# Kernel tuning notes

Measured on AMD Instinct MI355X. Metric: run time of the kernel, lower is better.

## Reference

```python
import jax, jax.numpy as jnp
import numpy as np

NUM_HEAD = 8


def setup_inputs() -> dict:
    key = jax.random.key(0)
    ks = jax.random.split(key, 4)
    B, nd, nh, nw, N, C = 1, 4, 4, 4, 512, 512
    x = jax.random.normal(ks[0], (B, nd, nh, nw, N, C), dtype=jnp.float32)
    w_qkv = jax.random.normal(ks[1], (C, 3 * C), dtype=jnp.float32) / np.sqrt(C).astype(np.float32)
    b_qkv = jnp.zeros((3 * C,), dtype=jnp.float32)
    w_proj = jax.random.normal(ks[2], (C, C), dtype=jnp.float32) / np.sqrt(C).astype(np.float32)
    b_proj = jnp.zeros((C,), dtype=jnp.float32)
    return {"x": x, "w_qkv": w_qkv, "b_qkv": b_qkv, "w_proj": w_proj, "b_proj": b_proj}


def reference(x, w_qkv, b_qkv, w_proj, b_proj):
    B, nd, nh, nw, N, C = x.shape
    hd = C // NUM_HEAD
    # QKV projection, split into q/k/v with per-head layout [B,nd,nh,nw,N,H,hd]
    qkv = (x @ w_qkv + b_qkv).reshape(B, nd, nh, nw, N, 3, NUM_HEAD, hd)
    q = qkv[..., 0, :, :]
    k = qkv[..., 1, :, :]
    v = qkv[..., 2, :, :]
    # Block-local attention. NOTE: original module defines self.scale but never
    # applies it in forward, so no 1/sqrt(hd) scaling here (faithful to source).
    attn = jnp.einsum('...qhd,...khd->...hqk', q, k)  # [B,nd,nh,nw,H,N,N]
    attn = jax.nn.softmax(attn, axis=-1)
    out = jnp.einsum('...hqk,...khd->...qhd', attn, v)  # [B,nd,nh,nw,N,H,hd]
    out = out.reshape(B, nd, nh, nw, N, C)
    return out @ w_proj + b_proj
```

## Files before the change

kernel.cpp:

```cpp
#include <hip/hip_runtime.h>
#include <hip/hip_bf16.h>

typedef _Float16 half8_t __attribute__((ext_vector_type(8)));
typedef _Float16 half4_t __attribute__((ext_vector_type(4)));
typedef _Float16 half2_t __attribute__((ext_vector_type(2)));
typedef float    f32x4   __attribute__((ext_vector_type(4)));
typedef float    f32x16  __attribute__((ext_vector_type(16)));

#define CDIM 512
#define NHEAD 8
#define HD 64
#define NTOK 512
#define NWIN 64
#define TC 1536

__device__ __forceinline__ float fexp2(float x) {
  float r;
  asm("v_exp_f32 %0, %1" : "=v"(r) : "v"(x));
  return r;
}

#define GLL16(g, l)                                                        \
  __builtin_amdgcn_global_load_lds((const __attribute__((address_space(1))) void*)(g), \
                                   (__attribute__((address_space(3))) void*)(l), 16, 0, 0)


__global__ __launch_bounds__(256) void cvt_x(const float* __restrict__ x,
                                             _Float16* __restrict__ x16, int n8) {
  int idx = blockIdx.x * 256 + threadIdx.x;
  if (idx < n8) {
    int row = (idx * 8) >> 9;
    int k = (idx * 8) & 511;
    const float4 v0 = *(const float4*)(x + (size_t)row * 512 + k);
    const float4 v1 = *(const float4*)(x + (size_t)row * 512 + k + 4);
    half8_t hv = {(_Float16)v0.x, (_Float16)v0.y, (_Float16)v0.z, (_Float16)v0.w,
                  (_Float16)v1.x, (_Float16)v1.y, (_Float16)v1.z, (_Float16)v1.w};
    *(half8_t*)(x16 + (size_t)(row >> 4) * 8192 + (size_t)(k >> 5) * 512 +
                (row & 15) * 32 + ((k & 31) >> 3) * 8) = hv;
  }
}

__global__ __launch_bounds__(256) void prep_weights(
    const float* __restrict__ wqkv, const float* __restrict__ wproj,
    _Float16* __restrict__ wqkvT, _Float16* __restrict__ wprojT) {
  __shared__ _Float16 T[64 * 65];
  int b = blockIdx.x;
  const float* src; _Float16* dst; int Cc, r0, c0; bool blocked;
  if (b < 192) {
    src = wqkv; dst = wqkvT; Cc = 1536; blocked = true;
    c0 = (b % 24) * 64; r0 = (b / 24) * 64;
  } else {
    b -= 192; src = wproj; dst = wprojT; Cc = 512; blocked = false;
    c0 = (b & 7) * 64; r0 = (b >> 3) * 64;
  }
  const int t = threadIdx.x;
#pragma unroll
  for (int i = 0; i < 16; ++i) {
    int idx = i * 256 + t, rr = idx >> 6, cc = idx & 63;
    T[rr * 65 + cc] = (_Float16)src[(size_t)(r0 + rr) * Cc + c0 + cc];
  }
  __syncthreads();
#pragma unroll
  for (int i = 0; i < 2; ++i) {
    int idx = i * 256 + t, ol = idx >> 3, c8 = idx & 7;
    half8_t vv;
#pragma unroll
    for (int e = 0; e < 8; ++e) vv[e] = T[(c8 * 8 + e) * 65 + ol];
    int o = c0 + ol, k = r0 + c8 * 8;
    if (blocked)
      *(half8_t*)(dst + (size_t)(o >> 4) * 8192 + (size_t)(k >> 5) * 512 +
                  (o & 15) * 32 + ((k & 31) >> 3) * 8) = vv;
    else
      *(half8_t*)(dst + (size_t)o * 512 + k) = vv;
  }
}

__global__ __launch_bounds__(256, 3) void gemm1_qkv(
    const _Float16* __restrict__ x16,
    const _Float16* __restrict__ wT,
    const float* __restrict__ bias,
    _Float16* __restrict__ qkv) {
  __shared__ __align__(16) char ring[3 * 16384];
  char* ringB = ring;
  const int tid = threadIdx.x;
  const int l = tid & 63;
  const int wid = tid >> 6;
  const int wr = wid >> 1, wc = wid & 1;
  const int lr = l & 15, g = l >> 4;
  const int koff = ((g ^ ((lr >> 1) & 3)) << 4);
  const int m0 = blockIdx.x * 128;
  const int cb = blockIdx.y * 128;
  const int j = cb >> 9;

  const int r4 = l >> 2;
  const int schk = (l & 3) ^ ((r4 >> 1) & 3);
  const size_t laneT = (size_t)r4 * 64 + (size_t)schk * 16;
  const size_t aTile = ((size_t)(blockIdx.x * 8 + wid * 2)) * 16384 + laneT;
  const size_t bTile = ((size_t)(blockIdx.y * 8 + wid * 2)) * 16384 + laneT;

#define ISSUE_G1(KS)                                                              \
  {                                                                               \
    char* sa = ringB + ((KS) % 3) * 16384;                                        \
    char* sbB = sa + 8192;                                                        \
    _Pragma("unroll") for (int i = 0; i < 2; ++i) {                               \
      GLL16((const char*)x16 + aTile + (size_t)i * 16384 + (size_t)(KS)*1024,     \
            sa + wid * 2048 + i * 1024);                                          \
      GLL16((const char*)wT + bTile + (size_t)i * 16384 + (size_t)(KS)*1024,      \
            sbB + wid * 2048 + i * 1024);                                         \
    }                                                                             \
  }

  ISSUE_G1(0) ISSUE_G1(1)

  f32x4 acc[4][4] = {};

#define GITER(KS, NW)                                                             \
  {                                                                               \
    asm volatile("s_waitcnt vmcnt(" NW ")" ::: "memory");                         \
    __builtin_amdgcn_sched_barrier(0);                                            \
    asm volatile("s_barrier" ::: "memory");                                       \
    if ((KS) + 2 < 16) ISSUE_G1((KS) + 2)                                         \
    char* sa = ringB + ((KS) % 3) * 16384;                                        \
    char* sbB = sa + 8192;                                                        \
    half8_t a[4], b[4];                                                           \
    _Pragma("unroll") for (int mt = 0; mt < 4; ++mt)                              \
        a[mt] = *(const half8_t*)(sa + (wr * 64 + mt * 16 + lr) * 64 + koff);     \
    _Pragma("unroll") for (int nt = 0; nt < 4; ++nt)                              \
        b[nt] = *(const half8_t*)(sbB + (wc * 64 + nt * 16 + lr) * 64 + koff);    \
    __builtin_amdgcn_s_setprio(1);                                                \
    _Pragma("unroll") for (int mt = 0; mt < 4; ++mt)                              \
        _Pragma("unroll") for (int nt = 0; nt < 4; ++nt)                          \
            acc[mt][nt] =                                                         \
                __builtin_amdgcn_mfma_f32_16x16x32_f16(a[mt], b[nt], acc[mt][nt], 0, 0, 0); \
    __builtin_amdgcn_s_setprio(0);                                                \
  }

  GITER(0, "4")  GITER(1, "4")  GITER(2, "4")  GITER(3, "4")
  GITER(4, "4")  GITER(5, "4")  GITER(6, "4")  GITER(7, "4")
  GITER(8, "4")  GITER(9, "4")  GITER(10, "4") GITER(11, "4")
  GITER(12, "4") GITER(13, "4") GITER(14, "4") GITER(15, "0")

  if (j == 2) {
#pragma unroll
    for (int nt = 0; nt < 4; ++nt) {
      const int ch = cb + wc * 64 + nt * 16 + lr;
      const int h = (ch >> 6) & 7, d = ch & 63;
      const float bvs = bias[ch];
#pragma unroll
      for (int mt = 0; mt < 4; ++mt) {
        const int row = m0 + wr * 64 + mt * 16 + g * 4;
        const int wL = row >> 9, n = row & 511;
        _Float16* panel = qkv + ((size_t)(wL * 24 + 16 + h) << 15);
        const int kg = n >> 4, hh = (n >> 2) & 1, e4 = (n & 8) >> 1;
        half4_t pk = {(_Float16)(acc[mt][nt][0] + bvs), (_Float16)(acc[mt][nt][1] + bvs),
                      (_Float16)(acc[mt][nt][2] + bvs), (_Float16)(acc[mt][nt][3] + bvs)};
        *(half4_t*)(panel + ((size_t)(kg * 2 + hh) * 64 + d) * 8 + e4) = pk;
      }
    }
  } else {
    __syncthreads();
    const float scl = (j == 0) ? 1.44269504f : 1.0f;
    char* CB = ringB;
#pragma unroll
    for (int nt = 0; nt < 4; ++nt) {
      const int chl = wc * 64 + nt * 16 + lr;
      const float bvs = bias[cb + chl];
#pragma unroll
      for (int mt = 0; mt < 4; ++mt) {
#pragma unroll
        for (int r = 0; r < 4; ++r) {
          int nl = wr * 64 + mt * 16 + g * 4 + r;
          *(_Float16*)(CB + nl * 256 + ((chl * 2) ^ ((nl & 7) << 5))) =
              (_Float16)((acc[mt][nt][r] + bvs) * scl);
        }
      }
    }
    __syncthreads();
#pragma unroll
    for (int i = 0; i < 8; ++i) {
      int idx = i * 256 + tid, nl = idx >> 4, c8 = idx & 15;
      half8_t vv = *(const half8_t*)(CB + nl * 256 + ((c8 * 16) ^ ((nl & 7) << 5)));
      int chg = cb + c8 * 8;
      int h = (chg >> 6) & 7, d = chg & 63;
      int ng = m0 + nl, wL = ng >> 9, nn = ng & 511;
      _Float16* panel = qkv + ((size_t)(wL * 24 + j * 8 + h) << 15);
      *(half8_t*)(panel + (size_t)nn * 64 + d) = vv;
    }
  }
}

__global__ __launch_bounds__(512) void attn_win(_Float16* __restrict__ qkv) {
  __shared__ __align__(16) char ring[4 * 8192];
  char* ringB = ring;
  const int tid = threadIdx.x;
  const int l = tid & 63;
  const int wid = tid >> 6;
  const int q32 = l & 31;
  const int h2 = l >> 5;
  const int wh = blockIdx.x;
  const int qc = blockIdx.y;
  const int h = wh & 7;
  const int w = wh >> 3;
  _Float16* Qp = qkv + ((size_t)(w * 24 + h) << 15);
  const _Float16* Kp = qkv + ((size_t)(w * 24 + 8 + h) << 15);
  const _Float16* Vp = qkv + ((size_t)(w * 24 + 16 + h) << 15);
  const int qrow = qc * 256 + wid * 32 + q32;

  const size_t kSrc = (size_t)(l >> 3) * 128 + (size_t)((l & 7) ^ (l >> 3)) * 16;
  const int kof0 = ((0 * 2 + h2) ^ (q32 & 7)) << 4;
  const int kof1 = ((1 * 2 + h2) ^ (q32 & 7)) << 4;
  const int kof2 = ((2 * 2 + h2) ^ (q32 & 7)) << 4;
  const int kof3 = ((3 * 2 + h2) ^ (q32 & 7)) << 4;
  const int voff = 4096 + h2 * 1024 + q32 * 16;

#define ISSUE_SLOT(KT)                                                            \
  {                                                                               \
    char* sb = ringB + ((KT)&3) * 8192;                                           \
    if (wid < 4) {                                                                \
      GLL16((const char*)Kp + (size_t)(KT)*4096 + (size_t)wid * 1024 + kSrc,      \
            sb + wid * 1024);                                                     \
    } else {                                                                      \
      GLL16((const char*)Vp + (size_t)(KT)*4096 + (size_t)(wid - 4) * 1024 + l * 16, \
            sb + 4096 + (wid - 4) * 1024);                                        \
    }                                                                             \
  }

  half8_t qf[4];
#pragma unroll
  for (int j = 0; j < 4; ++j)
    qf[j] = *(const half8_t*)(Qp + (size_t)qrow * 64 + j * 16 + h2 * 8);
  asm volatile("s_waitcnt vmcnt(0)" ::: "memory");

  ISSUE_SLOT(0) ISSUE_SLOT(1) ISSUE_SLOT(2)

  f32x16 o0 = {}, o1 = {};
  float m_run = -1e30f, lsum = 0.f;

#define AITER(KT, NW)                                                             \
  {                                                                               \
    asm volatile("s_waitcnt vmcnt(" NW ")" ::: "memory");                         \
    __builtin_amdgcn_sched_barrier(0);                                            \
    asm volatile("s_barrier" ::: "memory");                                       \
    if ((KT) + 3 < 16) ISSUE_SLOT((KT) + 3)                                       \
    char* sl = ringB + ((KT)&3) * 8192;                                           \
    half8_t kf0 = *(const half8_t*)(sl + q32 * 128 + kof0);                       \
    half8_t kf1 = *(const half8_t*)(sl + q32 * 128 + kof1);                       \
    half8_t kf2 = *(const half8_t*)(sl + q32 * 128 + kof2);                       \
    half8_t kf3 = *(const half8_t*)(sl + q32 * 128 + kof3);                       \
    __builtin_amdgcn_s_setprio(1);                                                \
    f32x16 s = {};                                                                \
    s = __builtin_amdgcn_mfma_f32_32x32x16_f16(kf0, qf[0], s, 0, 0, 0);           \
    s = __builtin_amdgcn_mfma_f32_32x32x16_f16(kf1, qf[1], s, 0, 0, 0);           \
    s = __builtin_amdgcn_mfma_f32_32x32x16_f16(kf2, qf[2], s, 0, 0, 0);           \
    s = __builtin_amdgcn_mfma_f32_32x32x16_f16(kf3, qf[3], s, 0, 0, 0);           \
    __builtin_amdgcn_s_setprio(0);                                                \
    float ma = fmaxf(fmaxf(s[0], s[1]), s[2]);                                    \
    float mb = fmaxf(fmaxf(s[3], s[4]), s[5]);                                    \
    float mc = fmaxf(fmaxf(s[6], s[7]), s[8]);                                    \
    float md = fmaxf(fmaxf(s[9], s[10]), s[11]);                                  \
    float me = fmaxf(fmaxf(s[12], s[13]), s[14]);                                 \
    float mf_ = fmaxf(fmaxf(ma, mb), mc);                                         \
    float mg = fmaxf(fmaxf(md, me), s[15]);                                       \
    float tmax = fmaxf(mf_, mg);                                                  \
    tmax = fmaxf(tmax, __shfl_xor(tmax, 32));                                     \
    if (!__all(tmax <= m_run + 11.5f)) {                                          \
      float mNew = fmaxf(m_run, tmax);                                            \
      float sc = fexp2(m_run - mNew);                                             \
      lsum *= sc;                                                                 \
      _Pragma("unroll") for (int r = 0; r < 16; ++r) { o0[r] *= sc; o1[r] *= sc; }\
      m_run = mNew;                                                               \
    }                                                                             \
    half8_t pf0, pf1;                                                             \
    float tsum = 0.f;                                                             \
    _Pragma("unroll") for (int e = 0; e < 4; ++e) {                               \
      float a0 = fexp2(s[2 * e] - m_run), a1 = fexp2(s[2 * e + 1] - m_run);       \
      tsum += a0 + a1;                                                            \
      ((half2_t*)&pf0)[e] =                                                       \
          __builtin_bit_cast(half2_t, __builtin_amdgcn_cvt_pkrtz(a0, a1));        \
    }                                                                             \
    _Pragma("unroll") for (int e = 0; e < 4; ++e) {                               \
      float a0 = fexp2(s[8 + 2 * e] - m_run), a1 = fexp2(s[9 + 2 * e] - m_run);   \
      tsum += a0 + a1;                                                            \
      ((half2_t*)&pf1)[e] =                                                       \
          __builtin_bit_cast(half2_t, __builtin_amdgcn_cvt_pkrtz(a0, a1));        \
    }                                                                             \
    tsum += __shfl_xor(tsum, 32);                                                 \
    lsum += tsum;                                                                 \
    half8_t vf0 = *(const half8_t*)(sl + voff);                                   \
    half8_t vf1 = *(const half8_t*)(sl + voff + 512);                             \
    half8_t vf2 = *(const half8_t*)(sl + voff + 2048);                            \
    half8_t vf3 = *(const half8_t*)(sl + voff + 2560);                            \
    __builtin_amdgcn_s_setprio(1);                                                \
    o0 = __builtin_amdgcn_mfma_f32_32x32x16_f16(vf0, pf0, o0, 0, 0, 0);           \
    o1 = __builtin_amdgcn_mfma_f32_32x32x16_f16(vf1, pf0, o1, 0, 0, 0);           \
    o0 = __builtin_amdgcn_mfma_f32_32x32x16_f16(vf2, pf1, o0, 0, 0, 0);           \
    o1 = __builtin_amdgcn_mfma_f32_32x32x16_f16(vf3, pf1, o1, 0, 0, 0);           \
    __builtin_amdgcn_s_setprio(0);                                                \
  }

  AITER(0, "2")  AITER(1, "2")  AITER(2, "2")  AITER(3, "2")
  AITER(4, "2")  AITER(5, "2")  AITER(6, "2")  AITER(7, "2")
  AITER(8, "2")  AITER(9, "2")  AITER(10, "2") AITER(11, "2")
  AITER(12, "2") AITER(13, "2") AITER(14, "1") AITER(15, "0")

  const float inv = 1.0f / lsum;
#pragma unroll
  for (int rq = 0; rq < 4; ++rq) {
    half4_t v0, v1;
#pragma unroll
    for (int i = 0; i < 4; ++i) {
      v0[i] = (_Float16)(o0[rq * 4 + i] * inv);
      v1[i] = (_Float16)(o1[rq * 4 + i] * inv);
    }
    *(half4_t*)(Qp + (size_t)qrow * 64 + 8 * rq + 4 * h2) = v0;
    *(half4_t*)(Qp + (size_t)qrow * 64 + 32 + 8 * rq + 4 * h2) = v1;
  }
}

__global__ __launch_bounds__(256) void gemm2_proj(
    const _Float16* __restrict__ qkv,
    const _Float16* __restrict__ wpT,
    const float* __restrict__ bias,
    float* __restrict__ out) {
  const int tid = threadIdx.x, l = tid & 63;
  const int wid = tid >> 6, wr = wid >> 1, wc = wid & 1;
  const int lr = l & 15, lk8 = (l >> 4) * 8;
  const int m0 = blockIdx.x * 128, n0 = blockIdx.y * 128;
  size_t aBase[4];
#pragma unroll
  for (int mt = 0; mt < 4; ++mt) {
    int row = m0 + wr * 64 + mt * 16 + lr;
    int wL = row >> 9, n = row & 511;
    aBase[mt] = ((size_t)(wL * 24) << 15) + (size_t)n * 64 + lk8;
  }
  size_t bBase[4];
#pragma unroll
  for (int nt = 0; nt < 4; ++nt)
    bBase[nt] = (size_t)(n0 + wc * 64 + nt * 16 + lr) * 512 + lk8;

  half8_t a[4], b[4];
#pragma unroll
  for (int mt = 0; mt < 4; ++mt) a[mt] = *(const half8_t*)(qkv + aBase[mt]);
#pragma unroll
  for (int nt = 0; nt < 4; ++nt) b[nt] = *(const half8_t*)(wpT + bBase[nt]);

  f32x4 acc[4][4] = {};
#pragma unroll 2
  for (int ks = 0; ks < 16; ++ks) {
    half8_t an[4], bn[4];
    if (ks < 15) {
      const size_t aoff = (size_t)((ks + 1) >> 1) * 32768 + (size_t)((ks + 1) & 1) * 32;
#pragma unroll
      for (int mt = 0; mt < 4; ++mt) an[mt] = *(const half8_t*)(qkv + aBase[mt] + aoff);
#pragma unroll
      for (int nt = 0; nt < 4; ++nt) bn[nt] = *(const half8_t*)(wpT + bBase[nt] + (ks + 1) * 32);
    }
#pragma unroll
    for (int mt = 0; mt < 4; ++mt)
#pragma unroll
      for (int nt = 0; nt < 4; ++nt)
        acc[mt][nt] = __builtin_amdgcn_mfma_f32_16x16x32_f16(a[mt], b[nt], acc[mt][nt], 0, 0, 0);
#pragma unroll
    for (int i = 0; i < 4; ++i) { a[i] = an[i]; b[i] = bn[i]; }
  }
#pragma unroll
  for (int nt = 0; nt < 4; ++nt) {
    int col = n0 + wc * 64 + nt * 16 + lr;
    float bv = bias[col];
#pragma unroll
    for (int mt = 0; mt < 4; ++mt) {
      int row = m0 + wr * 64 + mt * 16 + ((l >> 4) << 2);
#pragma unroll
      for (int r = 0; r < 4; ++r)
        out[(size_t)(row + r) * 512 + col] = acc[mt][nt][r] + bv;
    }
  }
}

extern "C" void kernel_launch(void* const* d_in, const int* in_sizes, int n_in,
                              void* d_out, int out_size, void* d_ws, size_t ws_size,
                              hipStream_t stream) {
  const float* x = (const float*)d_in[0];
  const float* wqkv = (const float*)d_in[1];
  const float* bqkv = (const float*)d_in[2];
  const float* wproj = (const float*)d_in[3];
  const float* bproj = (const float*)d_in[4];
  float* out = (float*)d_out;

  _Float16* wqkvT = (_Float16*)d_ws;
  _Float16* wprojT = wqkvT + (size_t)TC * CDIM;
  _Float16* chunkws = wprojT + (size_t)CDIM * CDIM;
  const size_t fixed = ((size_t)TC * CDIM + (size_t)CDIM * CDIM) * sizeof(_Float16);
  const size_t perwin = ((size_t)NTOK * CDIM + (size_t)24 * 32768) * sizeof(_Float16);
  int nw = 64;
  while (nw > 1 && fixed + (size_t)nw * perwin > ws_size) nw >>= 1;

  prep_weights<<<dim3(256), 256, 0, stream>>>(wqkv, wproj, wqkvT, wprojT);
  for (int wbase = 0; wbase < NWIN; wbase += nw) {
    const float* xc = x + (size_t)wbase * NTOK * CDIM;
    float* oc = out + (size_t)wbase * NTOK * CDIM;
    _Float16* x16 = chunkws;
    _Float16* qkvws = chunkws + (size_t)nw * NTOK * CDIM;
    const int n8 = nw * NTOK * CDIM / 8;
    cvt_x<<<dim3((n8 + 255) / 256), 256, 0, stream>>>(xc, x16, n8);
    gemm1_qkv<<<dim3(nw * 4, 12), 256, 0, stream>>>(x16, wqkvT, bqkv, qkvws);
    attn_win<<<dim3(nw * 8, 2), 512, 0, stream>>>(qkvws);
    gemm2_proj<<<dim3(nw * 4, 4), 256, 0, stream>>>(qkvws, wprojT, bproj, oc);
  }
}
```

Measured before the change: 222.3 us.

## Process two query tiles per wave in attention; restructure x conversion per row block

The attention kernel now has each wave handle 64 query rows (two 32-row tiles) across the full 512-query window. This halves the grid and reuses each K/V LDS fragment for twice as many MFMAs, which halves redundant K/V loads per window. The cost is doubled accumulator register pressure and fewer blocks to fill the GPU (512 instead of 1024). The x conversion kernel is also remapped so each block converts one 16-row slab with a loop.

```diff
diff --git a/kernel.cpp b/kernel.cpp
--- a/kernel.cpp
+++ b/kernel.cpp
@@ -26,17 +26,20 @@
 
 
 __global__ __launch_bounds__(256) void cvt_x(const float* __restrict__ x,
-                                             _Float16* __restrict__ x16, int n8) {
-  int idx = blockIdx.x * 256 + threadIdx.x;
-  if (idx < n8) {
-    int row = (idx * 8) >> 9;
-    int k = (idx * 8) & 511;
-    const float4 v0 = *(const float4*)(x + (size_t)row * 512 + k);
-    const float4 v1 = *(const float4*)(x + (size_t)row * 512 + k + 4);
+                                             _Float16* __restrict__ x16) {
+  const int rb = blockIdx.x;
+  const int l = threadIdx.x & 63, wv = threadIdx.x >> 6;
+  const int r4 = l >> 2, c = l & 3;
+  const float* src = x + (size_t)rb * 16 * 512 + (size_t)r4 * 512;
+  _Float16* dst = x16 + (size_t)rb * 8192;
+#pragma unroll
+  for (int i = 0; i < 4; ++i) {
+    int ks = wv * 4 + i;
+    const float4 v0 = *(const float4*)(src + ks * 32 + c * 8);
+    const float4 v1 = *(const float4*)(src + ks * 32 + c * 8 + 4);
     half8_t hv = {(_Float16)v0.x, (_Float16)v0.y, (_Float16)v0.z, (_Float16)v0.w,
                   (_Float16)v1.x, (_Float16)v1.y, (_Float16)v1.z, (_Float16)v1.w};
-    *(half8_t*)(x16 + (size_t)(row >> 4) * 8192 + (size_t)(k >> 5) * 512 +
-                (row & 15) * 32 + ((k & 31) >> 3) * 8) = hv;
+    *(half8_t*)(dst + ks * 512 + r4 * 32 + c * 8) = hv;
   }
 }
 
@@ -198,13 +201,13 @@
   const int q32 = l & 31;
   const int h2 = l >> 5;
   const int wh = blockIdx.x;
-  const int qc = blockIdx.y;
   const int h = wh & 7;
   const int w = wh >> 3;
   _Float16* Qp = qkv + ((size_t)(w * 24 + h) << 15);
   const _Float16* Kp = qkv + ((size_t)(w * 24 + 8 + h) << 15);
   const _Float16* Vp = qkv + ((size_t)(w * 24 + 16 + h) << 15);
-  const int qrow = qc * 256 + wid * 32 + q32;
+  const int qrowA = wid * 64 + q32;
+  const int qrowB = qrowA + 32;
 
   const size_t kSrc = (size_t)(l >> 3) * 128 + (size_t)((l & 7) ^ (l >> 3)) * 16;
   const int kof0 = ((0 * 2 + h2) ^ (q32 & 7)) << 4;
@@ -225,16 +228,28 @@
     }                                                                             \
   }
 
-  half8_t qf[4];
-#pragma unroll
-  for (int j = 0; j < 4; ++j)
-    qf[j] = *(const half8_t*)(Qp + (size_t)qrow * 64 + j * 16 + h2 * 8);
+  half8_t qfA0, qfA1, qfA2, qfA3, qfB0, qfB1, qfB2, qfB3;
+  qfA0 = *(const half8_t*)(Qp + (size_t)qrowA * 64 + 0 * 16 + h2 * 8);
+  qfA1 = *(const half8_t*)(Qp + (size_t)qrowA * 64 + 1 * 16 + h2 * 8);
+  qfA2 = *(const half8_t*)(Qp + (size_t)qrowA * 64 + 2 * 16 + h2 * 8);
+  qfA3 = *(const half8_t*)(Qp + (size_t)qrowA * 64 + 3 * 16 + h2 * 8);
+  qfB0 = *(const half8_t*)(Qp + (size_t)qrowB * 64 + 0 * 16 + h2 * 8);
+  qfB1 = *(const half8_t*)(Qp + (size_t)qrowB * 64 + 1 * 16 + h2 * 8);
+  qfB2 = *(const half8_t*)(Qp + (size_t)qrowB * 64 + 2 * 16 + h2 * 8);
+  qfB3 = *(const half8_t*)(Qp + (size_t)qrowB * 64 + 3 * 16 + h2 * 8);
   asm volatile("s_waitcnt vmcnt(0)" ::: "memory");
 
   ISSUE_SLOT(0) ISSUE_SLOT(1) ISSUE_SLOT(2)
 
-  f32x16 o0 = {}, o1 = {};
-  float m_run = -1e30f, lsum = 0.f;
+  f32x16 oA0 = {}, oA1 = {}, oB0 = {}, oB1 = {};
+  float mA = -1e30f, lsA = 0.f, mB = -1e30f, lsB = 0.f;
+
+#define SMAX(s)                                                                   \
+  fmaxf(fmaxf(fmaxf(fmaxf(fmaxf(s[0], s[1]), s[2]),                               \
+                    fmaxf(fmaxf(s[3], s[4]), s[5])),                              \
+              fmaxf(fmaxf(s[6], s[7]), s[8])),                                    \
+        fmaxf(fmaxf(fmaxf(s[9], s[10]), s[11]),                                   \
+              fmaxf(fmaxf(s[12], s[13]), fmaxf(s[14], s[15]))))
 
 #define AITER(KT, NW)                                                             \
   {                                                                               \
@@ -248,53 +263,77 @@
     half8_t kf2 = *(const half8_t*)(sl + q32 * 128 + kof2);                       \
     half8_t kf3 = *(const half8_t*)(sl + q32 * 128 + kof3);                       \
     __builtin_amdgcn_s_setprio(1);                                                \
-    f32x16 s = {};                                                                \
-    s = __builtin_amdgcn_mfma_f32_32x32x16_f16(kf0, qf[0], s, 0, 0, 0);           \
-    s = __builtin_amdgcn_mfma_f32_32x32x16_f16(kf1, qf[1], s, 0, 0, 0);           \
-    s = __builtin_amdgcn_mfma_f32_32x32x16_f16(kf2, qf[2], s, 0, 0, 0);           \
-    s = __builtin_amdgcn_mfma_f32_32x32x16_f16(kf3, qf[3], s, 0, 0, 0);           \
+    f32x16 sA = {}, sB = {};                                                      \
+    sA = __builtin_amdgcn_mfma_f32_32x32x16_f16(kf0, qfA0, sA, 0, 0, 0);          \
+    sB = __builtin_amdgcn_mfma_f32_32x32x16_f16(kf0, qfB0, sB, 0, 0, 0);          \
+    sA = __builtin_amdgcn_mfma_f32_32x32x16_f16(kf1, qfA1, sA, 0, 0, 0);          \
+    sB = __builtin_amdgcn_mfma_f32_32x32x16_f16(kf1, qfB1, sB, 0, 0, 0);          \
+    sA = __builtin_amdgcn_mfma_f32_32x32x16_f16(kf2, qfA2, sA, 0, 0, 0);          \
+    sB = __builtin_amdgcn_mfma_f32_32x32x16_f16(kf2, qfB2, sB, 0, 0, 0);          \
+    sA = __builtin_amdgcn_mfma_f32_32x32x16_f16(kf3, qfA3, sA, 0, 0, 0);          \
+    sB = __builtin_amdgcn_mfma_f32_32x32x16_f16(kf3, qfB3, sB, 0, 0, 0);          \
     __builtin_amdgcn_s_setprio(0);                                                \
-    float ma = fmaxf(fmaxf(s[0], s[1]), s[2]);                                    \
-    float mb = fmaxf(fmaxf(s[3], s[4]), s[5]);                                    \
-    float mc = fmaxf(fmaxf(s[6], s[7]), s[8]);                                    \
-    float md = fmaxf(fmaxf(s[9], s[10]), s[11]);                                  \
-    float me = fmaxf(fmaxf(s[12], s[13]), s[14]);                                 \
-    float mf_ = fmaxf(fmaxf(ma, mb), mc);                                         \
-    float mg = fmaxf(fmaxf(md, me), s[15]);                                       \
-    float tmax = fmaxf(mf_, mg);                                                  \
-    tmax = fmaxf(tmax, __shfl_xor(tmax, 32));                                     \
-    if (!__all(tmax <= m_run + 11.5f)) {                                          \
-      float mNew = fmaxf(m_run, tmax);                                            \
-      float sc = fexp2(m_run - mNew);                                             \
-      lsum *= sc;                                                                 \
-      _Pragma("unroll") for (int r = 0; r < 16; ++r) { o0[r] *= sc; o1[r] *= sc; }\
-      m_run = mNew;                                                               \
-    }                                                                             \
-    half8_t pf0, pf1;                                                             \
-    float tsum = 0.f;                                                             \
+    float tmaxA = SMAX(sA);                                                       \
+    tmaxA = fmaxf(tmaxA, __shfl_xor(tmaxA, 32));                                  \
+    if (!__all(tmaxA <= mA + 11.5f)) {                                            \
+      float mN = fmaxf(mA, tmaxA);                                                \
+      float sc = fexp2(mA - mN);                                                  \
+      lsA *= sc;                                                                  \
+      _Pragma("unroll") for (int r = 0; r < 16; ++r) { oA0[r] *= sc; oA1[r] *= sc; } \
+      mA = mN;                                                                    \
+    }                                                                             \
+    float tmaxB = SMAX(sB);                                                       \
+    tmaxB = fmaxf(tmaxB, __shfl_xor(tmaxB, 32));                                  \
+    if (!__all(tmaxB <= mB + 11.5f)) {                                            \
+      float mN = fmaxf(mB, tmaxB);                                                \
+      float sc = fexp2(mB - mN);                                                  \
+      lsB *= sc;                                                                  \
+      _Pragma("unroll") for (int r = 0; r < 16; ++r) { oB0[r] *= sc; oB1[r] *= sc; } \
+      mB = mN;                                                                    \
+    }                                                                             \
+    half8_t pfA0, pfA1, pfB0, pfB1;                                               \
+    float tsA = 0.f, tsB = 0.f;                                                   \
     _Pragma("unroll") for (int e = 0; e < 4; ++e) {                               \
-      float a0 = fexp2(s[2 * e] - m_run), a1 = fexp2(s[2 * e + 1] - m_run);       \
-      tsum += a0 + a1;                                                            \
-      ((half2_t*)&pf0)[e] =                                                       \
+      float a0 = fexp2(sA[2 * e] - mA), a1 = fexp2(sA[2 * e + 1] - mA);           \
+      tsA += a0 + a1;                                                             \
+      ((half2_t*)&pfA0)[e] =                                                      \
           __builtin_bit_cast(half2_t, __builtin_amdgcn_cvt_pkrtz(a0, a1));        \
     }                                                                             \
     _Pragma("unroll") for (int e = 0; e < 4; ++e) {                               \
-      float a0 = fexp2(s[8 + 2 * e] - m_run), a1 = fexp2(s[9 + 2 * e] - m_run);   \
-      tsum += a0 + a1;                                                            \
-      ((half2_t*)&pf1)[e] =                                                       \
+      float a0 = fexp2(sA[8 + 2 * e] - mA), a1 = fexp2(sA[9 + 2 * e] - mA);       \
+      tsA += a0 + a1;                                                             \
+      ((half2_t*)&pfA1)[e] =                                                      \
           __builtin_bit_cast(half2_t, __builtin_amdgcn_cvt_pkrtz(a0, a1));        \
     }                                                                             \
-    tsum += __shfl_xor(tsum, 32);                                                 \
-    lsum += tsum;                                                                 \
+    _Pragma("unroll") for (int e = 0; e < 4; ++e) {                               \
+      float a0 = fexp2(sB[2 * e] - mB), a1 = fexp2(sB[2 * e + 1] - mB);           \
+      tsB += a0 + a1;                                                             \
+      ((half2_t*)&pfB0)[e] =                                                      \
+          __builtin_bit_cast(half2_t, __builtin_amdgcn_cvt_pkrtz(a0, a1));        \
+    }                                                                             \
+    _Pragma("unroll") for (int e = 0; e < 4; ++e) {                               \
+      float a0 = fexp2(sB[8 + 2 * e] - mB), a1 = fexp2(sB[9 + 2 * e] - mB);       \
+      tsB += a0 + a1;                                                             \
+      ((half2_t*)&pfB1)[e] =                                                      \
+          __builtin_bit_cast(half2_t, __builtin_amdgcn_cvt_pkrtz(a0, a1));        \
+    }                                                                             \
+    tsA += __shfl_xor(tsA, 32);                                                   \
+    lsA += tsA;                                                                   \
+    tsB += __shfl_xor(tsB, 32);                                                   \
+    lsB += tsB;                                                                   \
     half8_t vf0 = *(const half8_t*)(sl + voff);                                   \
     half8_t vf1 = *(const half8_t*)(sl + voff + 512);                             \
     half8_t vf2 = *(const half8_t*)(sl + voff + 2048);                            \
     half8_t vf3 = *(const half8_t*)(sl + voff + 2560);                            \
     __builtin_amdgcn_s_setprio(1);                                                \
-    o0 = __builtin_amdgcn_mfma_f32_32x32x16_f16(vf0, pf0, o0, 0, 0, 0);           \
-    o1 = __builtin_amdgcn_mfma_f32_32x32x16_f16(vf1, pf0, o1, 0, 0, 0);           \
-    o0 = __builtin_amdgcn_mfma_f32_32x32x16_f16(vf2, pf1, o0, 0, 0, 0);           \
-    o1 = __builtin_amdgcn_mfma_f32_32x32x16_f16(vf3, pf1, o1, 0, 0, 0);           \
+    oA0 = __builtin_amdgcn_mfma_f32_32x32x16_f16(vf0, pfA0, oA0, 0, 0, 0);        \
+    oB0 = __builtin_amdgcn_mfma_f32_32x32x16_f16(vf0, pfB0, oB0, 0, 0, 0);        \
+    oA1 = __builtin_amdgcn_mfma_f32_32x32x16_f16(vf1, pfA0, oA1, 0, 0, 0);        \
+    oB1 = __builtin_amdgcn_mfma_f32_32x32x16_f16(vf1, pfB0, oB1, 0, 0, 0);        \
+    oA0 = __builtin_amdgcn_mfma_f32_32x32x16_f16(vf2, pfA1, oA0, 0, 0, 0);        \
+    oB0 = __builtin_amdgcn_mfma_f32_32x32x16_f16(vf2, pfB1, oB0, 0, 0, 0);        \
+    oA1 = __builtin_amdgcn_mfma_f32_32x32x16_f16(vf3, pfA1, oA1, 0, 0, 0);        \
+    oB1 = __builtin_amdgcn_mfma_f32_32x32x16_f16(vf3, pfB1, oB1, 0, 0, 0);        \
     __builtin_amdgcn_s_setprio(0);                                                \
   }
 
@@ -303,17 +342,22 @@
   AITER(8, "2")  AITER(9, "2")  AITER(10, "2") AITER(11, "2")
   AITER(12, "2") AITER(13, "2") AITER(14, "1") AITER(15, "0")
 
-  const float inv = 1.0f / lsum;
+  const float invA = 1.0f / lsA;
+  const float invB = 1.0f / lsB;
 #pragma unroll
   for (int rq = 0; rq < 4; ++rq) {
-    half4_t v0, v1;
+    half4_t a0, a1, b0, b1;
 #pragma unroll
     for (int i = 0; i < 4; ++i) {
-      v0[i] = (_Float16)(o0[rq * 4 + i] * inv);
-      v1[i] = (_Float16)(o1[rq * 4 + i] * inv);
-    }
-    *(half4_t*)(Qp + (size_t)qrow * 64 + 8 * rq + 4 * h2) = v0;
-    *(half4_t*)(Qp + (size_t)qrow * 64 + 32 + 8 * rq + 4 * h2) = v1;
+      a0[i] = (_Float16)(oA0[rq * 4 + i] * invA);
+      a1[i] = (_Float16)(oA1[rq * 4 + i] * invA);
+      b0[i] = (_Float16)(oB0[rq * 4 + i] * invB);
+      b1[i] = (_Float16)(oB1[rq * 4 + i] * invB);
+    }
+    *(half4_t*)(Qp + (size_t)qrowA * 64 + 8 * rq + 4 * h2) = a0;
+    *(half4_t*)(Qp + (size_t)qrowA * 64 + 32 + 8 * rq + 4 * h2) = a1;
+    *(half4_t*)(Qp + (size_t)qrowB * 64 + 8 * rq + 4 * h2) = b0;
+    *(half4_t*)(Qp + (size_t)qrowB * 64 + 32 + 8 * rq + 4 * h2) = b1;
   }
 }
 
@@ -401,10 +445,9 @@
     float* oc = out + (size_t)wbase * NTOK * CDIM;
     _Float16* x16 = chunkws;
     _Float16* qkvws = chunkws + (size_t)nw * NTOK * CDIM;
-    const int n8 = nw * NTOK * CDIM / 8;
-    cvt_x<<<dim3((n8 + 255) / 256), 256, 0, stream>>>(xc, x16, n8);
+    cvt_x<<<dim3(nw * 32), 256, 0, stream>>>(xc, x16);
     gemm1_qkv<<<dim3(nw * 4, 12), 256, 0, stream>>>(x16, wqkvT, bqkv, qkvws);
-    attn_win<<<dim3(nw * 8, 2), 512, 0, stream>>>(qkvws);
+    attn_win<<<dim3(nw * 8), 512, 0, stream>>>(qkvws);
     gemm2_proj<<<dim3(nw * 4, 4), 256, 0, stream>>>(qkvws, wprojT, bproj, oc);
   }
 }
```

New measurement: 231.2 us. 4.0% more time.
